# Kernel optimization log

Hardware: AMD Instinct MI355X
Metric: run time of the kernel (lower is better)

Reference implementation:

```python
import jax, jax.numpy as jnp
import numpy as np

H = 6  # hidden size (hardcoded in module)

def _lstm_dir(xs, h0, c0, Wih, Whh, b, reverse):
    # xs: (T, B, D); Wih: (4H, D); Whh: (4H, H); b: (4H,) = b_ih + b_hh
    # PyTorch gate order: i, f, g, o
    def step(carry, xt):
        h, c = carry
        z = xt @ Wih.T + h @ Whh.T + b
        i, f, g, o = jnp.split(z, 4, axis=-1)
        c = jax.nn.sigmoid(f) * c + jax.nn.sigmoid(i) * jnp.tanh(g)
        h = jax.nn.sigmoid(o) * jnp.tanh(c)
        return (h, c), h
    _, hs = jax.lax.scan(step, (h0, c0), xs, reverse=reverse)
    return hs  # (T, B, H); for reverse=True, hs[t] is the backward-dir output at time t (PyTorch convention)


def setup_inputs() -> dict:
    key = jax.random.key(0)
    ks = jax.random.split(key, 24)
    B, T = 8192, 512
    k = 1.0 / np.sqrt(H)  # PyTorch LSTM init scale
    u = lambda kk, shp: jax.random.uniform(kk, shp, jnp.float32, -k, k)
    inp = {
        'time_feature': jax.random.normal(ks[0], (B, T, 6), jnp.float32),
        'h0': jax.random.uniform(ks[1], (4, B, H), jnp.float32),  # torch.rand in original
        'c0': jax.random.uniform(ks[2], (4, B, H), jnp.float32),
        # layer 0 (input dim 6): forward and reverse directions
        'Wih0f': u(ks[3], (4 * H, 6)),  'Whh0f': u(ks[4], (4 * H, H)),  'b0f': u(ks[5], (4 * H,)),
        'Wih0b': u(ks[6], (4 * H, 6)),  'Whh0b': u(ks[7], (4 * H, H)),  'b0b': u(ks[8], (4 * H,)),
        # layer 1 (input dim 12 = 2H): forward and reverse directions
        'Wih1f': u(ks[9], (4 * H, 2 * H)),  'Whh1f': u(ks[10], (4 * H, H)),  'b1f': u(ks[11], (4 * H,)),
        'Wih1b': u(ks[12], (4 * H, 2 * H)), 'Whh1b': u(ks[13], (4 * H, H)),  'b1b': u(ks[14], (4 * H,)),
        # final linear head: Linear(12, 6)
        'fc_w': u(ks[15], (H, 2 * H)), 'fc_b': u(ks[16], (H,)),
    }
    return inp


def reference(time_feature, h0, c0, Wih0f, Whh0f, b0f, Wih0b, Whh0b, b0b,
              Wih1f, Whh1f, b1f, Wih1b, Whh1b, b1b, fc_w, fc_b):
    # time_feature: (B, T, 6) -> time-major (T, B, 6)
    x = jnp.transpose(time_feature, (1, 0, 2))
    # layer 0, bidirectional (eval mode: inter-layer dropout disabled)
    f0 = _lstm_dir(x, h0[0], c0[0], Wih0f, Whh0f, b0f, reverse=False)
    r0 = _lstm_dir(x, h0[1], c0[1], Wih0b, Whh0b, b0b, reverse=True)
    l0 = jnp.concatenate([f0, r0], axis=-1)  # (T, B, 2H)
    # layer 1, bidirectional
    f1 = _lstm_dir(l0, h0[2], c0[2], Wih1f, Whh1f, b1f, reverse=False)
    r1 = _lstm_dir(l0, h0[3], c0[3], Wih1b, Whh1b, b1b, reverse=True)
    l1 = jnp.concatenate([f1, r1], axis=-1)  # (T, B, 2H)
    last = l1[-1]  # out[:, -1] in batch-first == last time step, (B, 2H)
    return jax.nn.relu(last) @ fc_w.T + fc_b  # (B, H)
```

## Files before the change

### kernel.cpp

```cpp
#include <hip/hip_runtime.h>

#define NB 8192
#define NT 512

typedef unsigned int u32;
typedef unsigned short u16;
typedef float f32x4 __attribute__((ext_vector_type(4)));
typedef u32 u32x2 __attribute__((ext_vector_type(2)));
typedef _Float16 h16x2 __attribute__((ext_vector_type(2)));

__device__ __forceinline__ float rcp_(float x){ return __builtin_amdgcn_rcpf(x); }
__device__ __forceinline__ float exp2_(float x){ return __builtin_amdgcn_exp2f(x); }
__device__ __forceinline__ float tanh_(float x){ return 1.0f - 2.0f*rcp_(1.0f + exp2_(2.88539008177792681f*x)); }
__device__ __forceinline__ float sigm(float x){ return rcp_(1.0f + exp2_(-1.44269504088896341f*x)); }

#define PINF(v)  asm volatile("" : "+v"(v))

template<int J>
__device__ __forceinline__ float swzbc(float x){
    return __int_as_float(__builtin_amdgcn_ds_swizzle(__float_as_int(x), (J<<5)|0x18));
}

__device__ __forceinline__ float upkh(u16 v){ _Float16 h; __builtin_memcpy(&h,&v,2); return (float)h; }
__device__ __forceinline__ float upk_lo(u32 v){ return upkh((u16)(v&0xffffu)); }
__device__ __forceinline__ float upk_hi(u32 v){ return upkh((u16)(v>>16)); }
__device__ __forceinline__ u32 pkrtz(float a, float b){
    auto p = __builtin_amdgcn_cvt_pkrtz(a, b);
    return __builtin_bit_cast(u32, p);
}
__device__ __forceinline__ float dot2f(h16x2 a, h16x2 b, float c){
#if __has_builtin(__builtin_amdgcn_fdot2)
    return __builtin_amdgcn_fdot2(a, b, c, false);
#else
    return fmaf((float)a.x, (float)b.x, fmaf((float)a.y, (float)b.y, c));
#endif
}
__device__ __forceinline__ float dot2u(u32 w, u32 d, float c){
    return dot2f(__builtin_bit_cast(h16x2, w), __builtin_bit_cast(h16x2, d), c);
}


__global__ __launch_bounds__(64)
__attribute__((amdgpu_waves_per_eu(2,2)))
void lstm_l0v2(
    const float* __restrict__ x,
    const float* __restrict__ h0, const float* __restrict__ c0,
    const float* __restrict__ Wf, const float* __restrict__ Uf, const float* __restrict__ bf,
    const float* __restrict__ Wb, const float* __restrict__ Ub, const float* __restrict__ bbv,
    char* __restrict__ fbuf, char* __restrict__ bbuf)
{
    const int l  = threadIdx.x;
    const int j  = l & 7;
    const int jj = (j < 6) ? j : (j - 2);
    const int e  = blockIdx.x*8 + (l >> 3);
    const int b  = e & (NB-1);
    const int dir = e >> 13;

    const float* W  = dir ? Wb  : Wf;
    const float* U  = dir ? Ub  : Uf;
    const float* bi = dir ? bbv : bf;

    u32 wd[4][6]; float cEb[4];
#pragma unroll
    for (int g=0; g<4; ++g){
        const int row = g*6 + jj;
        const float cs = (g==2) ? -2.88539008177792681f : -1.44269504088896341f;
#pragma unroll
        for (int k=0;k<3;++k) wd[g][k]   = pkrtz(cs*W[row*6+2*k], cs*W[row*6+2*k+1]);
#pragma unroll
        for (int k=0;k<3;++k) wd[g][3+k] = pkrtz(cs*U[row*6+2*k], cs*U[row*6+2*k+1]);
        cEb[g] = cs * bi[row];
    }
#pragma unroll
    for (int g=0; g<4; ++g){
#pragma unroll
        for (int k=0;k<6;++k) PINF(wd[g][k]);
        PINF(cEb[g]);
    }

    float cc = c0[dir*(NB*6) + b*6 + jj];
    float hn = h0[dir*(NB*6) + b*6 + jj];
    u32 d01, d23, d45;
    {
        const float t0=swzbc<0>(hn), t1=swzbc<1>(hn), t2=swzbc<2>(hn),
                    t3=swzbc<3>(hn), t4=swzbc<4>(hn), t5=swzbc<5>(hn);
        d01=pkrtz(t0,t1); d23=pkrtz(t2,t3); d45=pkrtz(t4,t5);
    }

    const char* xb = (const char*)(x + (size_t)b*(NT*6));
    char* obase = (dir ? bbuf : fbuf) + (size_t)b*24 + j*8;
    const size_t tstr = (size_t)NB*24;

    auto STEP = [&](u32 px0, u32 px1, u32 px2){
        float z0=cEb[0], z1=cEb[1], z2=cEb[2], z3=cEb[3];
        z0=dot2u(wd[0][0],px0,z0); z0=dot2u(wd[0][1],px1,z0); z0=dot2u(wd[0][2],px2,z0);
        z0=dot2u(wd[0][3],d01,z0); z0=dot2u(wd[0][4],d23,z0); z0=dot2u(wd[0][5],d45,z0);
        z1=dot2u(wd[1][0],px0,z1); z1=dot2u(wd[1][1],px1,z1); z1=dot2u(wd[1][2],px2,z1);
        z1=dot2u(wd[1][3],d01,z1); z1=dot2u(wd[1][4],d23,z1); z1=dot2u(wd[1][5],d45,z1);
        z2=dot2u(wd[2][0],px0,z2); z2=dot2u(wd[2][1],px1,z2); z2=dot2u(wd[2][2],px2,z2);
        z2=dot2u(wd[2][3],d01,z2); z2=dot2u(wd[2][4],d23,z2); z2=dot2u(wd[2][5],d45,z2);
        z3=dot2u(wd[3][0],px0,z3); z3=dot2u(wd[3][1],px1,z3); z3=dot2u(wd[3][2],px2,z3);
        z3=dot2u(wd[3][3],d01,z3); z3=dot2u(wd[3][4],d23,z3); z3=dot2u(wd[3][5],d45,z3);
        const float iv = rcp_(1.0f + exp2_(z0));
        const float fv = rcp_(1.0f + exp2_(z1));
        const float gv = fmaf(2.0f, rcp_(1.0f + exp2_(z2)), -1.0f);
        const float ov = rcp_(1.0f + exp2_(z3));
        cc = fmaf(fv, cc, iv*gv);
        hn = ov * tanh_(cc);
        const float t0=swzbc<0>(hn), t1=swzbc<1>(hn), t2=swzbc<2>(hn),
                    t3=swzbc<3>(hn), t4=swzbc<4>(hn), t5=swzbc<5>(hn);
        d01=pkrtz(t0,t1); d23=pkrtz(t2,t3); d45=pkrtz(t4,t5);
    };

    f32x4 xA[3], xB[3];
    auto ldg = [&](int p, f32x4* d){
        const f32x4* q = (const f32x4*)(xb + (size_t)p*48);
        d[0]=q[0]; d[1]=q[1]; d[2]=q[2];
    };

    auto GROUP = [&](const f32x4* d, int p){
        u32 e0,e1,e2,o0,o1,o2;
        if (!dir){
            STEP(pkrtz(d[0].x,d[0].y), pkrtz(d[0].z,d[0].w), pkrtz(d[1].x,d[1].y));
            e0=d01; e1=d23; e2=d45;
            STEP(pkrtz(d[1].z,d[1].w), pkrtz(d[2].x,d[2].y), pkrtz(d[2].z,d[2].w));
            o0=d01; o1=d23; o2=d45;
        } else {
            STEP(pkrtz(d[1].z,d[1].w), pkrtz(d[2].x,d[2].y), pkrtz(d[2].z,d[2].w));
            o0=d01; o1=d23; o2=d45;
            STEP(pkrtz(d[0].x,d[0].y), pkrtz(d[0].z,d[0].w), pkrtz(d[1].x,d[1].y));
            e0=d01; e1=d23; e2=d45;
        }
        if (j < 3){
            const u32 se = (j==0)?e0:((j==1)?e1:e2);
            const u32 so = (j==0)?o0:((j==1)?o1:o2);
            u32x2 v; v.x=se; v.y=so;
            *(u32x2*)(obase + (size_t)p*tstr) = v;
        }
    };

    const int dp = dir ? -1 : 1;
    int p = dir ? (NT/2-1) : 0;
    {
        int p1 = p+dp; p1 = p1<0?0:(p1>NT/2-1?NT/2-1:p1);
        ldg(p, xA); ldg(p1, xB);
    }
    for (int it=0; it<NT/2; it+=2){
        GROUP(xA, p);
        { int pn=p+2*dp; pn = pn<0?0:(pn>NT/2-1?NT/2-1:pn); ldg(pn, xA); }
        p += dp;
        GROUP(xB, p);
        { int pn=p+2*dp; pn = pn<0?0:(pn>NT/2-1?NT/2-1:pn); ldg(pn, xB); }
        p += dp;
    }
}

__global__ __launch_bounds__(64)
__attribute__((amdgpu_waves_per_eu(1,1)))
void lstm_l1v2(
    const char* __restrict__ fbuf, const char* __restrict__ bbuf,
    const float* __restrict__ h0, const float* __restrict__ c0,
    const float* __restrict__ W1f, const float* __restrict__ U1f, const float* __restrict__ b1f,
    const float* __restrict__ W1b, const float* __restrict__ U1b, const float* __restrict__ b1b,
    const float* __restrict__ fcw, const float* __restrict__ fcb,
    float* __restrict__ out)
{
    const int l  = threadIdx.x;
    const int j  = l & 7;
    const int jj = (j < 6) ? j : (j - 2);
    const int b  = blockIdx.x*8 + (l >> 3);

    u32 wd1[4][9]; float cEb[4];
#pragma unroll
    for (int g=0; g<4; ++g){
        const int row = g*6 + jj;
        const float cs = (g==2) ? -2.88539008177792681f : -1.44269504088896341f;
#pragma unroll
        for (int k=0;k<3;++k) wd1[g][k]   = pkrtz(cs*W1f[row*12+2*k],   cs*W1f[row*12+2*k+1]);
#pragma unroll
        for (int k=0;k<3;++k) wd1[g][3+k] = pkrtz(cs*W1f[row*12+6+2*k], cs*W1f[row*12+6+2*k+1]);
#pragma unroll
        for (int k=0;k<3;++k) wd1[g][6+k] = pkrtz(cs*U1f[row*6+2*k],    cs*U1f[row*6+2*k+1]);
        cEb[g] = cs * b1f[row];
    }
#pragma unroll
    for (int g=0; g<4; ++g){
#pragma unroll
        for (int k=0;k<9;++k) PINF(wd1[g][k]);
        PINF(cEb[g]);
    }

    float cc = c0[2*(NB*6) + b*6 + jj];
    float hn = h0[2*(NB*6) + b*6 + jj];
    u32 d01, d23, d45;
    {
        const float t0=swzbc<0>(hn), t1=swzbc<1>(hn), t2=swzbc<2>(hn),
                    t3=swzbc<3>(hn), t4=swzbc<4>(hn), t5=swzbc<5>(hn);
        d01=pkrtz(t0,t1); d23=pkrtz(t2,t3); d45=pkrtz(t4,t5);
    }

    const char* fp = fbuf + (size_t)b*24;
    const char* rp = bbuf + (size_t)b*24;
    const size_t tstr = (size_t)NB*24;

    auto STEP = [&](u32 f0d, u32 f1d, u32 f2d, u32 r0d, u32 r1d, u32 r2d){
        float z0=cEb[0], z1=cEb[1], z2=cEb[2], z3=cEb[3];
        z0=dot2u(wd1[0][0],f0d,z0); z0=dot2u(wd1[0][1],f1d,z0); z0=dot2u(wd1[0][2],f2d,z0);
        z0=dot2u(wd1[0][3],r0d,z0); z0=dot2u(wd1[0][4],r1d,z0); z0=dot2u(wd1[0][5],r2d,z0);
        z0=dot2u(wd1[0][6],d01,z0); z0=dot2u(wd1[0][7],d23,z0); z0=dot2u(wd1[0][8],d45,z0);
        z1=dot2u(wd1[1][0],f0d,z1); z1=dot2u(wd1[1][1],f1d,z1); z1=dot2u(wd1[1][2],f2d,z1);
        z1=dot2u(wd1[1][3],r0d,z1); z1=dot2u(wd1[1][4],r1d,z1); z1=dot2u(wd1[1][5],r2d,z1);
        z1=dot2u(wd1[1][6],d01,z1); z1=dot2u(wd1[1][7],d23,z1); z1=dot2u(wd1[1][8],d45,z1);
        z2=dot2u(wd1[2][0],f0d,z2); z2=dot2u(wd1[2][1],f1d,z2); z2=dot2u(wd1[2][2],f2d,z2);
        z2=dot2u(wd1[2][3],r0d,z2); z2=dot2u(wd1[2][4],r1d,z2); z2=dot2u(wd1[2][5],r2d,z2);
        z2=dot2u(wd1[2][6],d01,z2); z2=dot2u(wd1[2][7],d23,z2); z2=dot2u(wd1[2][8],d45,z2);
        z3=dot2u(wd1[3][0],f0d,z3); z3=dot2u(wd1[3][1],f1d,z3); z3=dot2u(wd1[3][2],f2d,z3);
        z3=dot2u(wd1[3][3],r0d,z3); z3=dot2u(wd1[3][4],r1d,z3); z3=dot2u(wd1[3][5],r2d,z3);
        z3=dot2u(wd1[3][6],d01,z3); z3=dot2u(wd1[3][7],d23,z3); z3=dot2u(wd1[3][8],d45,z3);
        const float iv = rcp_(1.0f + exp2_(z0));
        const float fv = rcp_(1.0f + exp2_(z1));
        const float gv = fmaf(2.0f, rcp_(1.0f + exp2_(z2)), -1.0f);
        const float ov = rcp_(1.0f + exp2_(z3));
        cc = fmaf(fv, cc, iv*gv);
        hn = ov * tanh_(cc);
        const float t0=swzbc<0>(hn), t1=swzbc<1>(hn), t2=swzbc<2>(hn),
                    t3=swzbc<3>(hn), t4=swzbc<4>(hn), t5=swzbc<5>(hn);
        d01=pkrtz(t0,t1); d23=pkrtz(t2,t3); d45=pkrtz(t4,t5);
    };

    u32x2 FA[3], RA[3], FB[3], RB[3];
    auto ldp = [&](int p, u32x2* F, u32x2* R){
        const u32x2* f = (const u32x2*)(fp + (size_t)p*tstr);
        const u32x2* r = (const u32x2*)(rp + (size_t)p*tstr);
        F[0]=f[0]; F[1]=f[1]; F[2]=f[2];
        R[0]=r[0]; R[1]=r[1]; R[2]=r[2];
    };
    auto GROUP = [&](const u32x2* F, const u32x2* R){
        STEP(F[0].x, F[1].x, F[2].x, R[0].x, R[1].x, R[2].x);
        STEP(F[0].y, F[1].y, F[2].y, R[0].y, R[1].y, R[2].y);
    };

    ldp(0, FA, RA); ldp(1, FB, RB);
    for (int p=0; p<NT/2; p+=2){
        GROUP(FA, RA);
        { int pn=p+2; pn = pn>NT/2-1?NT/2-1:pn; ldp(pn, FA, RA); }
        GROUP(FB, RB);
        { int pn=p+3; pn = pn>NT/2-1?NT/2-1:pn; ldp(pn, FB, RB); }
    }

    float v[12];
    {
        const char* f255 = fp + (size_t)(NT/2-1)*tstr;
        const char* r255 = rp + (size_t)(NT/2-1)*tstr;
#pragma unroll
        for (int k=0;k<3;++k){
            const u32 fd = *(const u32*)(f255 + k*8 + 4);
            const u32 rd = *(const u32*)(r255 + k*8 + 4);
            v[2*k]   = upk_lo(fd);  v[2*k+1]   = upk_hi(fd);
            v[6+2*k] = upk_lo(rd);  v[6+2*k+1] = upk_hi(rd);
        }
    }

    const int base3 = 3*(NB*6) + b*6;
    float hr6[6];
#pragma unroll
    for (int k=0;k<6;++k) hr6[k] = h0[base3 + k];
    float cr = c0[base3 + jj];

    float zr[4];
#pragma unroll
    for (int g=0; g<4; ++g){
        const int row = g*6 + jj;
        float acc = b1b[row];
#pragma unroll
        for (int k=0;k<12;++k) acc = fmaf(W1b[row*12+k], v[k], acc);
#pragma unroll
        for (int k=0;k<6;++k)  acc = fmaf(U1b[row*6+k], hr6[k], acc);
        zr[g] = acc;
    }
    {
        const float iv = sigm(zr[0]);
        const float fv = sigm(zr[1]);
        const float gv = tanh_(zr[2]);
        cr = fmaf(fv, cr, iv*gv);
    }
    const float hrv = sigm(zr[3]) * tanh_(cr);

    float u[12];
    u[0]=fmaxf(swzbc<0>(hn),0.f); u[1]=fmaxf(swzbc<1>(hn),0.f); u[2]=fmaxf(swzbc<2>(hn),0.f);
    u[3]=fmaxf(swzbc<3>(hn),0.f); u[4]=fmaxf(swzbc<4>(hn),0.f); u[5]=fmaxf(swzbc<5>(hn),0.f);
    u[6]=fmaxf(swzbc<0>(hrv),0.f); u[7]=fmaxf(swzbc<1>(hrv),0.f); u[8]=fmaxf(swzbc<2>(hrv),0.f);
    u[9]=fmaxf(swzbc<3>(hrv),0.f); u[10]=fmaxf(swzbc<4>(hrv),0.f); u[11]=fmaxf(swzbc<5>(hrv),0.f);
    if (j < 6){
        float acc = fcb[j];
#pragma unroll
        for (int k=0;k<12;++k) acc = fmaf(fcw[j*12+k], u[k], acc);
        out[b*6 + j] = acc;
    }
}

extern "C" void kernel_launch(void* const* d_in, const int* in_sizes, int n_in,
                              void* d_out, int out_size, void* d_ws, size_t ws_size,
                              hipStream_t stream)
{
    (void)in_sizes; (void)n_in; (void)out_size; (void)ws_size;
    const float* x    = (const float*)d_in[0];
    const float* h0   = (const float*)d_in[1];
    const float* c0   = (const float*)d_in[2];
    const float* W0f  = (const float*)d_in[3];
    const float* U0f  = (const float*)d_in[4];
    const float* b0f  = (const float*)d_in[5];
    const float* W0b  = (const float*)d_in[6];
    const float* U0b  = (const float*)d_in[7];
    const float* b0b  = (const float*)d_in[8];
    const float* W1f  = (const float*)d_in[9];
    const float* U1f  = (const float*)d_in[10];
    const float* b1f  = (const float*)d_in[11];
    const float* W1b  = (const float*)d_in[12];
    const float* U1b  = (const float*)d_in[13];
    const float* b1b  = (const float*)d_in[14];
    const float* fcw  = (const float*)d_in[15];
    const float* fcb  = (const float*)d_in[16];
    float* out = (float*)d_out;
    char* ws = (char*)d_ws;

    char* fbuf = ws;
    char* bbuf = ws + (size_t)(NT/2)*NB*24;

    lstm_l0v2<<<dim3(2048), dim3(64), 0, stream>>>(x, h0, c0, W0f, U0f, b0f, W0b, U0b, b0b, fbuf, bbuf);
    lstm_l1v2<<<dim3(1024), dim3(64), 0, stream>>>(fbuf, bbuf, h0, c0,
        W1f, U1f, b1f, W1b, U1b, b1b, fcw, fcb, out);
}
```

Baseline: 276.5 us.

## Merge layer-0 forward and backward directions into one wave with interleaved steps

The layer-0 kernel now has each wave run both the forward and backward recurrences for its batch rows, alternating steps between the two independent chains. The launch drops to half as many waves at one wave per EU. The goal is instruction-level parallelism: the latency of one direction's dependency chain (dot2, transcendental, swizzle) can be hidden by the other direction, in place of relying on a second wave per EU. In exchange, register use doubles and there are fewer waves available to hide memory latency.

```diff
diff --git a/kernel.cpp b/kernel.cpp
--- a/kernel.cpp
+++ b/kernel.cpp
@@ -41,8 +41,8 @@
 
 
 __global__ __launch_bounds__(64)
-__attribute__((amdgpu_waves_per_eu(2,2)))
-void lstm_l0v2(
+__attribute__((amdgpu_waves_per_eu(1,1)))
+void lstm_l0m(
     const float* __restrict__ x,
     const float* __restrict__ h0, const float* __restrict__ c0,
     const float* __restrict__ Wf, const float* __restrict__ Uf, const float* __restrict__ bf,
@@ -52,106 +52,123 @@
     const int l  = threadIdx.x;
     const int j  = l & 7;
     const int jj = (j < 6) ? j : (j - 2);
-    const int e  = blockIdx.x*8 + (l >> 3);
-    const int b  = e & (NB-1);
-    const int dir = e >> 13;
-
-    const float* W  = dir ? Wb  : Wf;
-    const float* U  = dir ? Ub  : Uf;
-    const float* bi = dir ? bbv : bf;
-
-    u32 wd[4][6]; float cEb[4];
+    const int b  = blockIdx.x*8 + (l >> 3);
+
+    u32 wdF[4][6], wdB[4][6]; float cEbF[4], cEbB[4];
 #pragma unroll
     for (int g=0; g<4; ++g){
         const int row = g*6 + jj;
         const float cs = (g==2) ? -2.88539008177792681f : -1.44269504088896341f;
 #pragma unroll
-        for (int k=0;k<3;++k) wd[g][k]   = pkrtz(cs*W[row*6+2*k], cs*W[row*6+2*k+1]);
-#pragma unroll
-        for (int k=0;k<3;++k) wd[g][3+k] = pkrtz(cs*U[row*6+2*k], cs*U[row*6+2*k+1]);
-        cEb[g] = cs * bi[row];
-    }
-#pragma unroll
-    for (int g=0; g<4; ++g){
-#pragma unroll
-        for (int k=0;k<6;++k) PINF(wd[g][k]);
-        PINF(cEb[g]);
-    }
-
-    float cc = c0[dir*(NB*6) + b*6 + jj];
-    float hn = h0[dir*(NB*6) + b*6 + jj];
-    u32 d01, d23, d45;
+        for (int k=0;k<3;++k){
+            wdF[g][k]   = pkrtz(cs*Wf[row*6+2*k], cs*Wf[row*6+2*k+1]);
+            wdF[g][3+k] = pkrtz(cs*Uf[row*6+2*k], cs*Uf[row*6+2*k+1]);
+            wdB[g][k]   = pkrtz(cs*Wb[row*6+2*k], cs*Wb[row*6+2*k+1]);
+            wdB[g][3+k] = pkrtz(cs*Ub[row*6+2*k], cs*Ub[row*6+2*k+1]);
+        }
+        cEbF[g] = cs * bf[row];
+        cEbB[g] = cs * bbv[row];
+    }
+#pragma unroll
+    for (int g=0; g<4; ++g){
+#pragma unroll
+        for (int k=0;k<6;++k){ PINF(wdF[g][k]); PINF(wdB[g][k]); }
+        PINF(cEbF[g]); PINF(cEbB[g]);
+    }
+
+    float ccF = c0[0*(NB*6) + b*6 + jj];
+    float hnF = h0[0*(NB*6) + b*6 + jj];
+    float ccB = c0[1*(NB*6) + b*6 + jj];
+    float hnB = h0[1*(NB*6) + b*6 + jj];
+    u32 dF01,dF23,dF45, dB01,dB23,dB45;
     {
-        const float t0=swzbc<0>(hn), t1=swzbc<1>(hn), t2=swzbc<2>(hn),
-                    t3=swzbc<3>(hn), t4=swzbc<4>(hn), t5=swzbc<5>(hn);
-        d01=pkrtz(t0,t1); d23=pkrtz(t2,t3); d45=pkrtz(t4,t5);
+        float t0=swzbc<0>(hnF), t1=swzbc<1>(hnF), t2=swzbc<2>(hnF),
+              t3=swzbc<3>(hnF), t4=swzbc<4>(hnF), t5=swzbc<5>(hnF);
+        dF01=pkrtz(t0,t1); dF23=pkrtz(t2,t3); dF45=pkrtz(t4,t5);
+        t0=swzbc<0>(hnB); t1=swzbc<1>(hnB); t2=swzbc<2>(hnB);
+        t3=swzbc<3>(hnB); t4=swzbc<4>(hnB); t5=swzbc<5>(hnB);
+        dB01=pkrtz(t0,t1); dB23=pkrtz(t2,t3); dB45=pkrtz(t4,t5);
     }
 
     const char* xb = (const char*)(x + (size_t)b*(NT*6));
-    char* obase = (dir ? bbuf : fbuf) + (size_t)b*24 + j*8;
+    char* ofb = fbuf + (size_t)b*24 + j*8;
+    char* obb = bbuf + (size_t)b*24 + j*8;
     const size_t tstr = (size_t)NB*24;
 
-    auto STEP = [&](u32 px0, u32 px1, u32 px2){
-        float z0=cEb[0], z1=cEb[1], z2=cEb[2], z3=cEb[3];
-        z0=dot2u(wd[0][0],px0,z0); z0=dot2u(wd[0][1],px1,z0); z0=dot2u(wd[0][2],px2,z0);
-        z0=dot2u(wd[0][3],d01,z0); z0=dot2u(wd[0][4],d23,z0); z0=dot2u(wd[0][5],d45,z0);
-        z1=dot2u(wd[1][0],px0,z1); z1=dot2u(wd[1][1],px1,z1); z1=dot2u(wd[1][2],px2,z1);
-        z1=dot2u(wd[1][3],d01,z1); z1=dot2u(wd[1][4],d23,z1); z1=dot2u(wd[1][5],d45,z1);
-        z2=dot2u(wd[2][0],px0,z2); z2=dot2u(wd[2][1],px1,z2); z2=dot2u(wd[2][2],px2,z2);
-        z2=dot2u(wd[2][3],d01,z2); z2=dot2u(wd[2][4],d23,z2); z2=dot2u(wd[2][5],d45,z2);
-        z3=dot2u(wd[3][0],px0,z3); z3=dot2u(wd[3][1],px1,z3); z3=dot2u(wd[3][2],px2,z3);
-        z3=dot2u(wd[3][3],d01,z3); z3=dot2u(wd[3][4],d23,z3); z3=dot2u(wd[3][5],d45,z3);
+    auto STEPF = [&](u32 px0, u32 px1, u32 px2){
+        float z0=cEbF[0], z1=cEbF[1], z2=cEbF[2], z3=cEbF[3];
+        z0=dot2u(wdF[0][0],px0,z0); z0=dot2u(wdF[0][1],px1,z0); z0=dot2u(wdF[0][2],px2,z0);
+        z0=dot2u(wdF[0][3],dF01,z0); z0=dot2u(wdF[0][4],dF23,z0); z0=dot2u(wdF[0][5],dF45,z0);
+        z1=dot2u(wdF[1][0],px0,z1); z1=dot2u(wdF[1][1],px1,z1); z1=dot2u(wdF[1][2],px2,z1);
+        z1=dot2u(wdF[1][3],dF01,z1); z1=dot2u(wdF[1][4],dF23,z1); z1=dot2u(wdF[1][5],dF45,z1);
+        z2=dot2u(wdF[2][0],px0,z2); z2=dot2u(wdF[2][1],px1,z2); z2=dot2u(wdF[2][2],px2,z2);
+        z2=dot2u(wdF[2][3],dF01,z2); z2=dot2u(wdF[2][4],dF23,z2); z2=dot2u(wdF[2][5],dF45,z2);
+        z3=dot2u(wdF[3][0],px0,z3); z3=dot2u(wdF[3][1],px1,z3); z3=dot2u(wdF[3][2],px2,z3);
+        z3=dot2u(wdF[3][3],dF01,z3); z3=dot2u(wdF[3][4],dF23,z3); z3=dot2u(wdF[3][5],dF45,z3);
         const float iv = rcp_(1.0f + exp2_(z0));
         const float fv = rcp_(1.0f + exp2_(z1));
         const float gv = fmaf(2.0f, rcp_(1.0f + exp2_(z2)), -1.0f);
         const float ov = rcp_(1.0f + exp2_(z3));
-        cc = fmaf(fv, cc, iv*gv);
-        hn = ov * tanh_(cc);
-        const float t0=swzbc<0>(hn), t1=swzbc<1>(hn), t2=swzbc<2>(hn),
-                    t3=swzbc<3>(hn), t4=swzbc<4>(hn), t5=swzbc<5>(hn);
-        d01=pkrtz(t0,t1); d23=pkrtz(t2,t3); d45=pkrtz(t4,t5);
-    };
-
-    f32x4 xA[3], xB[3];
+        ccF = fmaf(fv, ccF, iv*gv);
+        hnF = ov * tanh_(ccF);
+        const float t0=swzbc<0>(hnF), t1=swzbc<1>(hnF), t2=swzbc<2>(hnF),
+                    t3=swzbc<3>(hnF), t4=swzbc<4>(hnF), t5=swzbc<5>(hnF);
+        dF01=pkrtz(t0,t1); dF23=pkrtz(t2,t3); dF45=pkrtz(t4,t5);
+    };
+    auto STEPB = [&](u32 px0, u32 px1, u32 px2){
+        float z0=cEbB[0], z1=cEbB[1], z2=cEbB[2], z3=cEbB[3];
+        z0=dot2u(wdB[0][0],px0,z0); z0=dot2u(wdB[0][1],px1,z0); z0=dot2u(wdB[0][2],px2,z0);
+        z0=dot2u(wdB[0][3],dB01,z0); z0=dot2u(wdB[0][4],dB23,z0); z0=dot2u(wdB[0][5],dB45,z0);
+        z1=dot2u(wdB[1][0],px0,z1); z1=dot2u(wdB[1][1],px1,z1); z1=dot2u(wdB[1][2],px2,z1);
+        z1=dot2u(wdB[1][3],dB01,z1); z1=dot2u(wdB[1][4],dB23,z1); z1=dot2u(wdB[1][5],dB45,z1);
+        z2=dot2u(wdB[2][0],px0,z2); z2=dot2u(wdB[2][1],px1,z2); z2=dot2u(wdB[2][2],px2,z2);
+        z2=dot2u(wdB[2][3],dB01,z2); z2=dot2u(wdB[2][4],dB23,z2); z2=dot2u(wdB[2][5],dB45,z2);
+        z3=dot2u(wdB[3][0],px0,z3); z3=dot2u(wdB[3][1],px1,z3); z3=dot2u(wdB[3][2],px2,z3);
+        z3=dot2u(wdB[3][3],dB01,z3); z3=dot2u(wdB[3][4],dB23,z3); z3=dot2u(wdB[3][5],dB45,z3);
+        const float iv = rcp_(1.0f + exp2_(z0));
+        const float fv = rcp_(1.0f + exp2_(z1));
+        const float gv = fmaf(2.0f, rcp_(1.0f + exp2_(z2)), -1.0f);
+        const float ov = rcp_(1.0f + exp2_(z3));
+        ccB = fmaf(fv, ccB, iv*gv);
+        hnB = ov * tanh_(ccB);
+        const float t0=swzbc<0>(hnB), t1=swzbc<1>(hnB), t2=swzbc<2>(hnB),
+                    t3=swzbc<3>(hnB), t4=swzbc<4>(hnB), t5=swzbc<5>(hnB);
+        dB01=pkrtz(t0,t1); dB23=pkrtz(t2,t3); dB45=pkrtz(t4,t5);
+    };
+
+    f32x4 xFA[3], xFB[3], xBA[3], xBB[3];
     auto ldg = [&](int p, f32x4* d){
         const f32x4* q = (const f32x4*)(xb + (size_t)p*48);
         d[0]=q[0]; d[1]=q[1]; d[2]=q[2];
     };
 
-    auto GROUP = [&](const f32x4* d, int p){
-        u32 e0,e1,e2,o0,o1,o2;
-        if (!dir){
-            STEP(pkrtz(d[0].x,d[0].y), pkrtz(d[0].z,d[0].w), pkrtz(d[1].x,d[1].y));
-            e0=d01; e1=d23; e2=d45;
-            STEP(pkrtz(d[1].z,d[1].w), pkrtz(d[2].x,d[2].y), pkrtz(d[2].z,d[2].w));
-            o0=d01; o1=d23; o2=d45;
-        } else {
-            STEP(pkrtz(d[1].z,d[1].w), pkrtz(d[2].x,d[2].y), pkrtz(d[2].z,d[2].w));
-            o0=d01; o1=d23; o2=d45;
-            STEP(pkrtz(d[0].x,d[0].y), pkrtz(d[0].z,d[0].w), pkrtz(d[1].x,d[1].y));
-            e0=d01; e1=d23; e2=d45;
+    auto GROUP = [&](const f32x4* fd, const f32x4* bd, int pf, int pb){
+        STEPF(pkrtz(fd[0].x,fd[0].y), pkrtz(fd[0].z,fd[0].w), pkrtz(fd[1].x,fd[1].y));
+        const u32 fe0=dF01, fe1=dF23, fe2=dF45;
+        STEPB(pkrtz(bd[1].z,bd[1].w), pkrtz(bd[2].x,bd[2].y), pkrtz(bd[2].z,bd[2].w));
+        const u32 bo0=dB01, bo1=dB23, bo2=dB45;
+        STEPF(pkrtz(fd[1].z,fd[1].w), pkrtz(fd[2].x,fd[2].y), pkrtz(fd[2].z,fd[2].w));
+        STEPB(pkrtz(bd[0].x,bd[0].y), pkrtz(bd[0].z,bd[0].w), pkrtz(bd[1].x,bd[1].y));
+        if (j < 3){
+            const u32 fe = (j==0)?fe0:((j==1)?fe1:fe2);
+            const u32 fo = (j==0)?dF01:((j==1)?dF23:dF45);
+            u32x2 vf; vf.x=fe; vf.y=fo;
+            *(u32x2*)(ofb + (size_t)pf*tstr) = vf;
+            const u32 be = (j==0)?dB01:((j==1)?dB23:dB45);
+            const u32 bo = (j==0)?bo0:((j==1)?bo1:bo2);
+            u32x2 vb; vb.x=be; vb.y=bo;
+            *(u32x2*)(obb + (size_t)pb*tstr) = vb;
         }
-        if (j < 3){
-            const u32 se = (j==0)?e0:((j==1)?e1:e2);
-            const u32 so = (j==0)?o0:((j==1)?o1:o2);
-            u32x2 v; v.x=se; v.y=so;
-            *(u32x2*)(obase + (size_t)p*tstr) = v;
-        }
-    };
-
-    const int dp = dir ? -1 : 1;
-    int p = dir ? (NT/2-1) : 0;
-    {
-        int p1 = p+dp; p1 = p1<0?0:(p1>NT/2-1?NT/2-1:p1);
-        ldg(p, xA); ldg(p1, xB);
-    }
+    };
+
+    ldg(0, xFA); ldg(1, xFB); ldg(NT/2-1, xBA); ldg(NT/2-2, xBB);
     for (int it=0; it<NT/2; it+=2){
-        GROUP(xA, p);
-        { int pn=p+2*dp; pn = pn<0?0:(pn>NT/2-1?NT/2-1:pn); ldg(pn, xA); }
-        p += dp;
-        GROUP(xB, p);
-        { int pn=p+2*dp; pn = pn<0?0:(pn>NT/2-1?NT/2-1:pn); ldg(pn, xB); }
-        p += dp;
+        GROUP(xFA, xBA, it, NT/2-1-it);
+        { int pn=it+2;       if (pn>NT/2-1) pn=NT/2-1; ldg(pn, xFA);
+          int qn=NT/2-3-it;  if (qn<0) qn=0;           ldg(qn, xBA); }
+        GROUP(xFB, xBB, it+1, NT/2-2-it);
+        { int pn=it+3;       if (pn>NT/2-1) pn=NT/2-1; ldg(pn, xFB);
+          int qn=NT/2-4-it;  if (qn<0) qn=0;           ldg(qn, xBB); }
     }
 }
 
@@ -327,7 +344,7 @@
     char* fbuf = ws;
     char* bbuf = ws + (size_t)(NT/2)*NB*24;
 
-    lstm_l0v2<<<dim3(2048), dim3(64), 0, stream>>>(x, h0, c0, W0f, U0f, b0f, W0b, U0b, b0b, fbuf, bbuf);
+    lstm_l0m<<<dim3(1024), dim3(64), 0, stream>>>(x, h0, c0, W0f, U0f, b0f, W0b, U0b, b0b, fbuf, bbuf);
     lstm_l1v2<<<dim3(1024), dim3(64), 0, stream>>>(fbuf, bbuf, h0, c0,
         W1f, U1f, b1f, W1b, U1b, b1b, fcw, fcb, out);
 }
```

Measured after the change: 293.0 us. 1.06x slower.

## Fuse layer-0 forward LSTM into layer-1 forward kernel, drop forward buffer

Applied to the files above, without the earlier changes.

The layer-0 forward direction now runs inside the layer-1 kernel, step by step alongside the layer-1 forward recurrence, so its hidden state feeds layer 1 directly from registers. The first kernel now computes only the layer-0 backward direction, with half the blocks and one wave per EU. This removes the write and re-read of the forward intermediate buffer and gives the second kernel two independent recurrences to interleave for latency hiding. The cost is a longer per-step chain and more registers in the fused kernel, and lower occupancy in the first kernel.

```diff
diff --git a/kernel.cpp b/kernel.cpp
--- a/kernel.cpp
+++ b/kernel.cpp
@@ -41,24 +41,17 @@
 
 
 __global__ __launch_bounds__(64)
-__attribute__((amdgpu_waves_per_eu(2,2)))
-void lstm_l0v2(
+__attribute__((amdgpu_waves_per_eu(1,1)))
+void lstm_l0b(
     const float* __restrict__ x,
     const float* __restrict__ h0, const float* __restrict__ c0,
-    const float* __restrict__ Wf, const float* __restrict__ Uf, const float* __restrict__ bf,
     const float* __restrict__ Wb, const float* __restrict__ Ub, const float* __restrict__ bbv,
-    char* __restrict__ fbuf, char* __restrict__ bbuf)
+    char* __restrict__ bbuf)
 {
     const int l  = threadIdx.x;
     const int j  = l & 7;
     const int jj = (j < 6) ? j : (j - 2);
-    const int e  = blockIdx.x*8 + (l >> 3);
-    const int b  = e & (NB-1);
-    const int dir = e >> 13;
-
-    const float* W  = dir ? Wb  : Wf;
-    const float* U  = dir ? Ub  : Uf;
-    const float* bi = dir ? bbv : bf;
+    const int b  = blockIdx.x*8 + (l >> 3);
 
     u32 wd[4][6]; float cEb[4];
 #pragma unroll
@@ -66,10 +59,11 @@
         const int row = g*6 + jj;
         const float cs = (g==2) ? -2.88539008177792681f : -1.44269504088896341f;
 #pragma unroll
-        for (int k=0;k<3;++k) wd[g][k]   = pkrtz(cs*W[row*6+2*k], cs*W[row*6+2*k+1]);
-#pragma unroll
-        for (int k=0;k<3;++k) wd[g][3+k] = pkrtz(cs*U[row*6+2*k], cs*U[row*6+2*k+1]);
-        cEb[g] = cs * bi[row];
+        for (int k=0;k<3;++k){
+            wd[g][k]   = pkrtz(cs*Wb[row*6+2*k], cs*Wb[row*6+2*k+1]);
+            wd[g][3+k] = pkrtz(cs*Ub[row*6+2*k], cs*Ub[row*6+2*k+1]);
+        }
+        cEb[g] = cs * bbv[row];
     }
 #pragma unroll
     for (int g=0; g<4; ++g){
@@ -78,8 +72,8 @@
         PINF(cEb[g]);
     }
 
-    float cc = c0[dir*(NB*6) + b*6 + jj];
-    float hn = h0[dir*(NB*6) + b*6 + jj];
+    float cc = c0[1*(NB*6) + b*6 + jj];
+    float hn = h0[1*(NB*6) + b*6 + jj];
     u32 d01, d23, d45;
     {
         const float t0=swzbc<0>(hn), t1=swzbc<1>(hn), t2=swzbc<2>(hn),
@@ -88,7 +82,7 @@
     }
 
     const char* xb = (const char*)(x + (size_t)b*(NT*6));
-    char* obase = (dir ? bbuf : fbuf) + (size_t)b*24 + j*8;
+    char* obase = bbuf + (size_t)b*24 + j*8;
     const size_t tstr = (size_t)NB*24;
 
     auto STEP = [&](u32 px0, u32 px1, u32 px2){
@@ -119,47 +113,33 @@
     };
 
     auto GROUP = [&](const f32x4* d, int p){
-        u32 e0,e1,e2,o0,o1,o2;
-        if (!dir){
-            STEP(pkrtz(d[0].x,d[0].y), pkrtz(d[0].z,d[0].w), pkrtz(d[1].x,d[1].y));
-            e0=d01; e1=d23; e2=d45;
-            STEP(pkrtz(d[1].z,d[1].w), pkrtz(d[2].x,d[2].y), pkrtz(d[2].z,d[2].w));
-            o0=d01; o1=d23; o2=d45;
-        } else {
-            STEP(pkrtz(d[1].z,d[1].w), pkrtz(d[2].x,d[2].y), pkrtz(d[2].z,d[2].w));
-            o0=d01; o1=d23; o2=d45;
-            STEP(pkrtz(d[0].x,d[0].y), pkrtz(d[0].z,d[0].w), pkrtz(d[1].x,d[1].y));
-            e0=d01; e1=d23; e2=d45;
-        }
+        STEP(pkrtz(d[1].z,d[1].w), pkrtz(d[2].x,d[2].y), pkrtz(d[2].z,d[2].w));
+        const u32 o0=d01, o1=d23, o2=d45;
+        STEP(pkrtz(d[0].x,d[0].y), pkrtz(d[0].z,d[0].w), pkrtz(d[1].x,d[1].y));
         if (j < 3){
-            const u32 se = (j==0)?e0:((j==1)?e1:e2);
+            const u32 se = (j==0)?d01:((j==1)?d23:d45);
             const u32 so = (j==0)?o0:((j==1)?o1:o2);
             u32x2 v; v.x=se; v.y=so;
             *(u32x2*)(obase + (size_t)p*tstr) = v;
         }
     };
 
-    const int dp = dir ? -1 : 1;
-    int p = dir ? (NT/2-1) : 0;
-    {
-        int p1 = p+dp; p1 = p1<0?0:(p1>NT/2-1?NT/2-1:p1);
-        ldg(p, xA); ldg(p1, xB);
-    }
+    ldg(NT/2-1, xA); ldg(NT/2-2, xB);
     for (int it=0; it<NT/2; it+=2){
-        GROUP(xA, p);
-        { int pn=p+2*dp; pn = pn<0?0:(pn>NT/2-1?NT/2-1:pn); ldg(pn, xA); }
-        p += dp;
-        GROUP(xB, p);
-        { int pn=p+2*dp; pn = pn<0?0:(pn>NT/2-1?NT/2-1:pn); ldg(pn, xB); }
-        p += dp;
+        GROUP(xA, NT/2-1-it);
+        { int qn=NT/2-3-it; if (qn<0) qn=0; ldg(qn, xA); }
+        GROUP(xB, NT/2-2-it);
+        { int qn=NT/2-4-it; if (qn<0) qn=0; ldg(qn, xB); }
     }
 }
 
 __global__ __launch_bounds__(64)
 __attribute__((amdgpu_waves_per_eu(1,1)))
-void lstm_l1v2(
-    const char* __restrict__ fbuf, const char* __restrict__ bbuf,
+void lstm_f01(
+    const char* __restrict__ bbuf,
+    const float* __restrict__ x,
     const float* __restrict__ h0, const float* __restrict__ c0,
+    const float* __restrict__ W0f, const float* __restrict__ U0f, const float* __restrict__ b0f,
     const float* __restrict__ W1f, const float* __restrict__ U1f, const float* __restrict__ b1f,
     const float* __restrict__ W1b, const float* __restrict__ U1b, const float* __restrict__ b1b,
     const float* __restrict__ fcw, const float* __restrict__ fcb,
@@ -170,95 +150,129 @@
     const int jj = (j < 6) ? j : (j - 2);
     const int b  = blockIdx.x*8 + (l >> 3);
 
-    u32 wd1[4][9]; float cEb[4];
+    u32 wd0[4][6]; float cEb0[4];
+    u32 wd1[4][9]; float cEb1[4];
 #pragma unroll
     for (int g=0; g<4; ++g){
         const int row = g*6 + jj;
         const float cs = (g==2) ? -2.88539008177792681f : -1.44269504088896341f;
 #pragma unroll
-        for (int k=0;k<3;++k) wd1[g][k]   = pkrtz(cs*W1f[row*12+2*k],   cs*W1f[row*12+2*k+1]);
-#pragma unroll
-        for (int k=0;k<3;++k) wd1[g][3+k] = pkrtz(cs*W1f[row*12+6+2*k], cs*W1f[row*12+6+2*k+1]);
-#pragma unroll
-        for (int k=0;k<3;++k) wd1[g][6+k] = pkrtz(cs*U1f[row*6+2*k],    cs*U1f[row*6+2*k+1]);
-        cEb[g] = cs * b1f[row];
-    }
-#pragma unroll
-    for (int g=0; g<4; ++g){
+        for (int k=0;k<3;++k){
+            wd0[g][k]   = pkrtz(cs*W0f[row*6+2*k], cs*W0f[row*6+2*k+1]);
+            wd0[g][3+k] = pkrtz(cs*U0f[row*6+2*k], cs*U0f[row*6+2*k+1]);
+            wd1[g][k]   = pkrtz(cs*W1f[row*12+2*k],   cs*W1f[row*12+2*k+1]);
+            wd1[g][3+k] = pkrtz(cs*W1f[row*12+6+2*k], cs*W1f[row*12+6+2*k+1]);
+            wd1[g][6+k] = pkrtz(cs*U1f[row*6+2*k],    cs*U1f[row*6+2*k+1]);
+        }
+        cEb0[g] = cs * b0f[row];
+        cEb1[g] = cs * b1f[row];
+    }
+#pragma unroll
+    for (int g=0; g<4; ++g){
+#pragma unroll
+        for (int k=0;k<6;++k) PINF(wd0[g][k]);
 #pragma unroll
         for (int k=0;k<9;++k) PINF(wd1[g][k]);
-        PINF(cEb[g]);
-    }
-
-    float cc = c0[2*(NB*6) + b*6 + jj];
-    float hn = h0[2*(NB*6) + b*6 + jj];
-    u32 d01, d23, d45;
+        PINF(cEb0[g]); PINF(cEb1[g]);
+    }
+
+    float cc0 = c0[0*(NB*6) + b*6 + jj];
+    float hn0 = h0[0*(NB*6) + b*6 + jj];
+    float cc1 = c0[2*(NB*6) + b*6 + jj];
+    float hn1 = h0[2*(NB*6) + b*6 + jj];
+    u32 d001,d023,d045, d101,d123,d145;
     {
-        const float t0=swzbc<0>(hn), t1=swzbc<1>(hn), t2=swzbc<2>(hn),
-                    t3=swzbc<3>(hn), t4=swzbc<4>(hn), t5=swzbc<5>(hn);
-        d01=pkrtz(t0,t1); d23=pkrtz(t2,t3); d45=pkrtz(t4,t5);
-    }
-
-    const char* fp = fbuf + (size_t)b*24;
+        float t0=swzbc<0>(hn0), t1=swzbc<1>(hn0), t2=swzbc<2>(hn0),
+              t3=swzbc<3>(hn0), t4=swzbc<4>(hn0), t5=swzbc<5>(hn0);
+        d001=pkrtz(t0,t1); d023=pkrtz(t2,t3); d045=pkrtz(t4,t5);
+        t0=swzbc<0>(hn1); t1=swzbc<1>(hn1); t2=swzbc<2>(hn1);
+        t3=swzbc<3>(hn1); t4=swzbc<4>(hn1); t5=swzbc<5>(hn1);
+        d101=pkrtz(t0,t1); d123=pkrtz(t2,t3); d145=pkrtz(t4,t5);
+    }
+
+    const char* xb = (const char*)(x + (size_t)b*(NT*6));
     const char* rp = bbuf + (size_t)b*24;
     const size_t tstr = (size_t)NB*24;
 
-    auto STEP = [&](u32 f0d, u32 f1d, u32 f2d, u32 r0d, u32 r1d, u32 r2d){
-        float z0=cEb[0], z1=cEb[1], z2=cEb[2], z3=cEb[3];
-        z0=dot2u(wd1[0][0],f0d,z0); z0=dot2u(wd1[0][1],f1d,z0); z0=dot2u(wd1[0][2],f2d,z0);
-        z0=dot2u(wd1[0][3],r0d,z0); z0=dot2u(wd1[0][4],r1d,z0); z0=dot2u(wd1[0][5],r2d,z0);
-        z0=dot2u(wd1[0][6],d01,z0); z0=dot2u(wd1[0][7],d23,z0); z0=dot2u(wd1[0][8],d45,z0);
-        z1=dot2u(wd1[1][0],f0d,z1); z1=dot2u(wd1[1][1],f1d,z1); z1=dot2u(wd1[1][2],f2d,z1);
-        z1=dot2u(wd1[1][3],r0d,z1); z1=dot2u(wd1[1][4],r1d,z1); z1=dot2u(wd1[1][5],r2d,z1);
-        z1=dot2u(wd1[1][6],d01,z1); z1=dot2u(wd1[1][7],d23,z1); z1=dot2u(wd1[1][8],d45,z1);
-        z2=dot2u(wd1[2][0],f0d,z2); z2=dot2u(wd1[2][1],f1d,z2); z2=dot2u(wd1[2][2],f2d,z2);
-        z2=dot2u(wd1[2][3],r0d,z2); z2=dot2u(wd1[2][4],r1d,z2); z2=dot2u(wd1[2][5],r2d,z2);
-        z2=dot2u(wd1[2][6],d01,z2); z2=dot2u(wd1[2][7],d23,z2); z2=dot2u(wd1[2][8],d45,z2);
-        z3=dot2u(wd1[3][0],f0d,z3); z3=dot2u(wd1[3][1],f1d,z3); z3=dot2u(wd1[3][2],f2d,z3);
-        z3=dot2u(wd1[3][3],r0d,z3); z3=dot2u(wd1[3][4],r1d,z3); z3=dot2u(wd1[3][5],r2d,z3);
-        z3=dot2u(wd1[3][6],d01,z3); z3=dot2u(wd1[3][7],d23,z3); z3=dot2u(wd1[3][8],d45,z3);
+    auto STEP0 = [&](u32 px0, u32 px1, u32 px2){
+        float z0=cEb0[0], z1=cEb0[1], z2=cEb0[2], z3=cEb0[3];
+        z0=dot2u(wd0[0][0],px0,z0); z0=dot2u(wd0[0][1],px1,z0); z0=dot2u(wd0[0][2],px2,z0);
+        z0=dot2u(wd0[0][3],d001,z0); z0=dot2u(wd0[0][4],d023,z0); z0=dot2u(wd0[0][5],d045,z0);
+        z1=dot2u(wd0[1][0],px0,z1); z1=dot2u(wd0[1][1],px1,z1); z1=dot2u(wd0[1][2],px2,z1);
+        z1=dot2u(wd0[1][3],d001,z1); z1=dot2u(wd0[1][4],d023,z1); z1=dot2u(wd0[1][5],d045,z1);
+        z2=dot2u(wd0[2][0],px0,z2); z2=dot2u(wd0[2][1],px1,z2); z2=dot2u(wd0[2][2],px2,z2);
+        z2=dot2u(wd0[2][3],d001,z2); z2=dot2u(wd0[2][4],d023,z2); z2=dot2u(wd0[2][5],d045,z2);
+        z3=dot2u(wd0[3][0],px0,z3); z3=dot2u(wd0[3][1],px1,z3); z3=dot2u(wd0[3][2],px2,z3);
+        z3=dot2u(wd0[3][3],d001,z3); z3=dot2u(wd0[3][4],d023,z3); z3=dot2u(wd0[3][5],d045,z3);
         const float iv = rcp_(1.0f + exp2_(z0));
         const float fv = rcp_(1.0f + exp2_(z1));
         const float gv = fmaf(2.0f, rcp_(1.0f + exp2_(z2)), -1.0f);
         const float ov = rcp_(1.0f + exp2_(z3));
-        cc = fmaf(fv, cc, iv*gv);
-        hn = ov * tanh_(cc);
-        const float t0=swzbc<0>(hn), t1=swzbc<1>(hn), t2=swzbc<2>(hn),
-                    t3=swzbc<3>(hn), t4=swzbc<4>(hn), t5=swzbc<5>(hn);
-        d01=pkrtz(t0,t1); d23=pkrtz(t2,t3); d45=pkrtz(t4,t5);
-    };
-
-    u32x2 FA[3], RA[3], FB[3], RB[3];
-    auto ldp = [&](int p, u32x2* F, u32x2* R){
-        const u32x2* f = (const u32x2*)(fp + (size_t)p*tstr);
+        cc0 = fmaf(fv, cc0, iv*gv);
+        hn0 = ov * tanh_(cc0);
+        const float t0=swzbc<0>(hn0), t1=swzbc<1>(hn0), t2=swzbc<2>(hn0),
+                    t3=swzbc<3>(hn0), t4=swzbc<4>(hn0), t5=swzbc<5>(hn0);
+        d001=pkrtz(t0,t1); d023=pkrtz(t2,t3); d045=pkrtz(t4,t5);
+    };
+    auto STEP1 = [&](u32 r0d, u32 r1d, u32 r2d){
+        float z0=cEb1[0], z1=cEb1[1], z2=cEb1[2], z3=cEb1[3];
+        z0=dot2u(wd1[0][0],d001,z0); z0=dot2u(wd1[0][1],d023,z0); z0=dot2u(wd1[0][2],d045,z0);
+        z0=dot2u(wd1[0][3],r0d,z0); z0=dot2u(wd1[0][4],r1d,z0); z0=dot2u(wd1[0][5],r2d,z0);
+        z0=dot2u(wd1[0][6],d101,z0); z0=dot2u(wd1[0][7],d123,z0); z0=dot2u(wd1[0][8],d145,z0);
+        z1=dot2u(wd1[1][0],d001,z1); z1=dot2u(wd1[1][1],d023,z1); z1=dot2u(wd1[1][2],d045,z1);
+        z1=dot2u(wd1[1][3],r0d,z1); z1=dot2u(wd1[1][4],r1d,z1); z1=dot2u(wd1[1][5],r2d,z1);
+        z1=dot2u(wd1[1][6],d101,z1); z1=dot2u(wd1[1][7],d123,z1); z1=dot2u(wd1[1][8],d145,z1);
+        z2=dot2u(wd1[2][0],d001,z2); z2=dot2u(wd1[2][1],d023,z2); z2=dot2u(wd1[2][2],d045,z2);
+        z2=dot2u(wd1[2][3],r0d,z2); z2=dot2u(wd1[2][4],r1d,z2); z2=dot2u(wd1[2][5],r2d,z2);
+        z2=dot2u(wd1[2][6],d101,z2); z2=dot2u(wd1[2][7],d123,z2); z2=dot2u(wd1[2][8],d145,z2);
+        z3=dot2u(wd1[3][0],d001,z3); z3=dot2u(wd1[3][1],d023,z3); z3=dot2u(wd1[3][2],d045,z3);
+        z3=dot2u(wd1[3][3],r0d,z3); z3=dot2u(wd1[3][4],r1d,z3); z3=dot2u(wd1[3][5],r2d,z3);
+        z3=dot2u(wd1[3][6],d101,z3); z3=dot2u(wd1[3][7],d123,z3); z3=dot2u(wd1[3][8],d145,z3);
+        const float iv = rcp_(1.0f + exp2_(z0));
+        const float fv = rcp_(1.0f + exp2_(z1));
+        const float gv = fmaf(2.0f, rcp_(1.0f + exp2_(z2)), -1.0f);
+        const float ov = rcp_(1.0f + exp2_(z3));
+        cc1 = fmaf(fv, cc1, iv*gv);
+        hn1 = ov * tanh_(cc1);
+        const float t0=swzbc<0>(hn1), t1=swzbc<1>(hn1), t2=swzbc<2>(hn1),
+                    t3=swzbc<3>(hn1), t4=swzbc<4>(hn1), t5=swzbc<5>(hn1);
+        d101=pkrtz(t0,t1); d123=pkrtz(t2,t3); d145=pkrtz(t4,t5);
+    };
+
+    f32x4 xA[3], xB[3];
+    u32x2 RA[3], RB[3];
+    auto ldg = [&](int p, f32x4* d){
+        const f32x4* q = (const f32x4*)(xb + (size_t)p*48);
+        d[0]=q[0]; d[1]=q[1]; d[2]=q[2];
+    };
+    auto ldr = [&](int p, u32x2* R){
         const u32x2* r = (const u32x2*)(rp + (size_t)p*tstr);
-        F[0]=f[0]; F[1]=f[1]; F[2]=f[2];
         R[0]=r[0]; R[1]=r[1]; R[2]=r[2];
     };
-    auto GROUP = [&](const u32x2* F, const u32x2* R){
-        STEP(F[0].x, F[1].x, F[2].x, R[0].x, R[1].x, R[2].x);
-        STEP(F[0].y, F[1].y, F[2].y, R[0].y, R[1].y, R[2].y);
-    };
-
-    ldp(0, FA, RA); ldp(1, FB, RB);
+
+    auto GROUP = [&](const f32x4* d, const u32x2* R){
+        STEP0(pkrtz(d[0].x,d[0].y), pkrtz(d[0].z,d[0].w), pkrtz(d[1].x,d[1].y));
+        STEP1(R[0].x, R[1].x, R[2].x);
+        STEP0(pkrtz(d[1].z,d[1].w), pkrtz(d[2].x,d[2].y), pkrtz(d[2].z,d[2].w));
+        STEP1(R[0].y, R[1].y, R[2].y);
+    };
+
+    ldg(0, xA); ldr(0, RA);
+    ldg(1, xB); ldr(1, RB);
     for (int p=0; p<NT/2; p+=2){
-        GROUP(FA, RA);
-        { int pn=p+2; pn = pn>NT/2-1?NT/2-1:pn; ldp(pn, FA, RA); }
-        GROUP(FB, RB);
-        { int pn=p+3; pn = pn>NT/2-1?NT/2-1:pn; ldp(pn, FB, RB); }
+        GROUP(xA, RA);
+        { int pn=p+2; if (pn>NT/2-1) pn=NT/2-1; ldg(pn, xA); ldr(pn, RA); }
+        GROUP(xB, RB);
+        { int pn=p+3; if (pn>NT/2-1) pn=NT/2-1; ldg(pn, xB); ldr(pn, RB); }
     }
 
     float v[12];
-    {
-        const char* f255 = fp + (size_t)(NT/2-1)*tstr;
-        const char* r255 = rp + (size_t)(NT/2-1)*tstr;
-#pragma unroll
-        for (int k=0;k<3;++k){
-            const u32 fd = *(const u32*)(f255 + k*8 + 4);
-            const u32 rd = *(const u32*)(r255 + k*8 + 4);
-            v[2*k]   = upk_lo(fd);  v[2*k+1]   = upk_hi(fd);
-            v[6+2*k] = upk_lo(rd);  v[6+2*k+1] = upk_hi(rd);
-        }
+    v[0]=swzbc<0>(hn0); v[1]=swzbc<1>(hn0); v[2]=swzbc<2>(hn0);
+    v[3]=swzbc<3>(hn0); v[4]=swzbc<4>(hn0); v[5]=swzbc<5>(hn0);
+#pragma unroll
+    for (int k=0;k<3;++k){
+        v[6+2*k] = upk_lo(RB[k].y);
+        v[7+2*k] = upk_hi(RB[k].y);
     }
 
     const int base3 = 3*(NB*6) + b*6;
@@ -287,8 +301,8 @@
     const float hrv = sigm(zr[3]) * tanh_(cr);
 
     float u[12];
-    u[0]=fmaxf(swzbc<0>(hn),0.f); u[1]=fmaxf(swzbc<1>(hn),0.f); u[2]=fmaxf(swzbc<2>(hn),0.f);
-    u[3]=fmaxf(swzbc<3>(hn),0.f); u[4]=fmaxf(swzbc<4>(hn),0.f); u[5]=fmaxf(swzbc<5>(hn),0.f);
+    u[0]=fmaxf(swzbc<0>(hn1),0.f); u[1]=fmaxf(swzbc<1>(hn1),0.f); u[2]=fmaxf(swzbc<2>(hn1),0.f);
+    u[3]=fmaxf(swzbc<3>(hn1),0.f); u[4]=fmaxf(swzbc<4>(hn1),0.f); u[5]=fmaxf(swzbc<5>(hn1),0.f);
     u[6]=fmaxf(swzbc<0>(hrv),0.f); u[7]=fmaxf(swzbc<1>(hrv),0.f); u[8]=fmaxf(swzbc<2>(hrv),0.f);
     u[9]=fmaxf(swzbc<3>(hrv),0.f); u[10]=fmaxf(swzbc<4>(hrv),0.f); u[11]=fmaxf(swzbc<5>(hrv),0.f);
     if (j < 6){
@@ -324,10 +338,9 @@
     float* out = (float*)d_out;
     char* ws = (char*)d_ws;
 
-    char* fbuf = ws;
-    char* bbuf = ws + (size_t)(NT/2)*NB*24;
-
-    lstm_l0v2<<<dim3(2048), dim3(64), 0, stream>>>(x, h0, c0, W0f, U0f, b0f, W0b, U0b, b0b, fbuf, bbuf);
-    lstm_l1v2<<<dim3(1024), dim3(64), 0, stream>>>(fbuf, bbuf, h0, c0,
-        W1f, U1f, b1f, W1b, U1b, b1b, fcw, fcb, out);
-}
+    char* bbuf = ws;
+
+    lstm_l0b<<<dim3(1024), dim3(64), 0, stream>>>(x, h0, c0, W0b, U0b, b0b, bbuf);
+    lstm_f01<<<dim3(1024), dim3(64), 0, stream>>>(bbuf, x, h0, c0,
+        W0f, U0f, b0f, W1f, U1f, b1f, W1b, U1b, b1b, fcw, fcb, out);
+}
```

After: 286.5 us. 3.6% more time.
